# Optimization experiments

Measured on AMD Instinct MI355X. Metric: run time of the kernel, lower is better.

The kernel has to match this reference:

```python
import jax, jax.numpy as jnp
import numpy as np

N = 12288   # num_nodes
D = 128     # isize
K_TOP = 31  # k + 1, per top_k(similarities, self.k + 1)


def setup_inputs() -> dict:
    key = jax.random.key(0)
    features = jax.random.normal(key, (N, D), dtype=jnp.float32)
    eye = jnp.eye(D, dtype=jnp.float32)  # param_init: weight <- I, bias <- 0
    return {
        "features": features,
        "W1": eye,
        "b1": jnp.zeros((D,), jnp.float32),
        "W2": eye,
        "b2": jnp.zeros((D,), jnp.float32),
    }


def reference(features, W1, b1, W2, b2):
    # internal_forward: Linear -> ReLU -> Linear (nlayers=2, act='relu')
    h = jax.nn.relu(features @ W1.T + b1)
    h = h @ W2.T + b2
    # F.normalize(h, dim=1, p=2) with eps=1e-12
    hn = h / jnp.maximum(jnp.linalg.norm(h, axis=1, keepdims=True), 1e-12)
    # dense N x N cosine similarity
    sim = hn @ hn.T
    # top_k: keep top (k+1) entries per row, zero elsewhere; then apply_non_linearity='relu'
    vals, idx = jax.lax.top_k(sim, K_TOP)          # [N, K_TOP]
    rows = jnp.arange(sim.shape[0])[:, None]       # [N, 1]
    # relu(sim * mask) == scatter relu(top-k values) into a zero matrix
    out = jnp.zeros_like(sim).at[rows, idx].set(jax.nn.relu(vals))
    return out
```

## Files before the change

### kernel.cpp

```cpp
#include <hip/hip_runtime.h>
#include <stdint.h>
#include <math.h>

#define NN 12288
#define DD 128
#define KTOP 31
#define TILE 128
#define GB (NN / TILE)
#define TCAND 64
#define CCAP 128
#define FUSE_ROWS 6144

typedef __attribute__((ext_vector_type(8))) short bf16x8;
typedef __attribute__((ext_vector_type(4))) float f32x4;

__device__ __forceinline__ unsigned short f2bf(float x) {
  unsigned int u = __float_as_uint(x);
  u += 0x7fffu + ((u >> 16) & 1u);
  return (unsigned short)(u >> 16);
}

__device__ __forceinline__ unsigned umed3(unsigned a, unsigned b, unsigned c) {
  unsigned d;
  asm("v_med3_u32 %0, %1, %2, %3" : "=v"(d) : "v"(a), "v"(b), "v"(c));
  return d;
}

__global__ __launch_bounds__(128)
void wtrans_kernel(const float* __restrict__ W1, const float* __restrict__ W2,
                   float* __restrict__ W1T, float* __restrict__ W2T) {
  const int r = blockIdx.x, c = threadIdx.x;
  W1T[(size_t)c * DD + r] = W1[(size_t)r * DD + c];
  W2T[(size_t)c * DD + r] = W2[(size_t)r * DD + c];
}

__global__ __launch_bounds__(128)
void mlp_norm_kernel(const float* __restrict__ feat,
                     const float* __restrict__ W1T, const float* __restrict__ b1,
                     const float* __restrict__ W2T, const float* __restrict__ b2,
                     double* __restrict__ hn64, unsigned short* __restrict__ hnb) {
  __shared__ double bufA[8][DD];
  __shared__ double bufB[8][DD];
  __shared__ double mnorm[8];
  const int t = threadIdx.x;
  const int row0 = blockIdx.x * 8;

  #pragma unroll
  for (int rr = 0; rr < 8; ++rr)
    bufA[rr][t] = (double)feat[(size_t)(row0 + rr) * DD + t];
  __syncthreads();

  {
    double acc[8] = {0,0,0,0,0,0,0,0};
    for (int k = 0; k < DD; k += 2) {
      double w0 = (double)W1T[(size_t)k * DD + t];
      double w1 = (double)W1T[(size_t)(k + 1) * DD + t];
      #pragma unroll
      for (int rr = 0; rr < 8; ++rr) {
        double2 a2 = *(const double2*)(&bufA[rr][k]);
        acc[rr] = fma(w0, a2.x, acc[rr]);
        acc[rr] = fma(w1, a2.y, acc[rr]);
      }
    }
    double bb = (double)b1[t];
    #pragma unroll
    for (int rr = 0; rr < 8; ++rr)
      bufB[rr][t] = fmax(acc[rr] + bb, 0.0);
  }
  __syncthreads();
  {
    double acc[8] = {0,0,0,0,0,0,0,0};
    for (int k = 0; k < DD; k += 2) {
      double w0 = (double)W2T[(size_t)k * DD + t];
      double w1 = (double)W2T[(size_t)(k + 1) * DD + t];
      #pragma unroll
      for (int rr = 0; rr < 8; ++rr) {
        double2 a2 = *(const double2*)(&bufB[rr][k]);
        acc[rr] = fma(w0, a2.x, acc[rr]);
        acc[rr] = fma(w1, a2.y, acc[rr]);
      }
    }
    double bb = (double)b2[t];
    #pragma unroll
    for (int rr = 0; rr < 8; ++rr)
      bufA[rr][t] = acc[rr] + bb;
  }
  __syncthreads();

  const int lane = t & 63;
  const int w = t >> 6;
  #pragma unroll
  for (int r2 = 0; r2 < 4; ++r2) {
    int rr = w * 4 + r2;
    double x0 = bufA[rr][lane];
    double x1 = bufA[rr][lane + 64];
    double s = x0 * x0 + x1 * x1;
    #pragma unroll
    for (int d = 1; d < 64; d <<= 1)
      s += __shfl_xor(s, d);
    if (lane == 0) mnorm[rr] = fmax(sqrt(s), 1e-12);
  }
  __syncthreads();
  #pragma unroll
  for (int rr = 0; rr < 8; ++rr) {
    double v = bufA[rr][t] / mnorm[rr];
    hn64[(size_t)(row0 + rr) * DD + t] = v;
    hnb[(size_t)(row0 + rr) * DD + t] = f2bf((float)v);
  }
}

__device__ __forceinline__ int lunit(int c, int r, int q) {
  return c * 512 + r * 4 + ((q + (r >> 1)) & 3);
}

__global__ __launch_bounds__(256)
void gemm_kernel(const unsigned short* __restrict__ hnb,
                 unsigned short* __restrict__ simmat) {
  __shared__ __attribute__((aligned(16))) unsigned short At[16384];
  __shared__ __attribute__((aligned(16))) unsigned short Bt[16384];
  const int t = threadIdx.x;
  const int lane = t & 63;
  const int wv = t >> 6;
  const int bi = blockIdx.x / GB, bj = blockIdx.x % GB;
  const int r0 = bi * TILE, c0 = bj * TILE;

  #pragma unroll
  for (int i = 0; i < 8; ++i) {
    int u = i * 256 + t;
    int c = u >> 9, r = (u >> 2) & 127, g = u & 3;
    int q = (g - (r >> 1)) & 3;
    uint4 v = *(const uint4*)(hnb + (size_t)(r0 + r) * DD + c * 32 + q * 8);
    *(uint4*)(At + u * 8) = v;
  }
  #pragma unroll
  for (int i = 0; i < 8; ++i) {
    int u = i * 256 + t;
    int c = u >> 9, r = (u >> 2) & 127, g = u & 3;
    int q = (g - (r >> 1)) & 3;
    uint4 v = *(const uint4*)(hnb + (size_t)(c0 + r) * DD + c * 32 + q * 8);
    *(uint4*)(Bt + u * 8) = v;
  }
  __syncthreads();

  const int wr = (wv >> 1) * 64;
  const int wc = (wv & 1) * 64;
  const int m = lane & 15, quad = lane >> 4;

  f32x4 acc[4][4] = {};
  #pragma unroll
  for (int kc = 0; kc < 4; ++kc) {
    bf16x8 a[4], b[4];
    #pragma unroll
    for (int i = 0; i < 4; ++i)
      a[i] = *(const bf16x8*)(At + lunit(kc, wr + i * 16 + m, quad) * 8);
    #pragma unroll
    for (int j = 0; j < 4; ++j)
      b[j] = *(const bf16x8*)(Bt + lunit(kc, wc + j * 16 + m, quad) * 8);
    #pragma unroll
    for (int i = 0; i < 4; ++i)
      #pragma unroll
      for (int j = 0; j < 4; ++j)
        acc[i][j] = __builtin_amdgcn_mfma_f32_16x16x32_bf16(a[i], b[j], acc[i][j], 0, 0, 0);
  }

  const bool evenl = !(lane & 1);
  #pragma unroll
  for (int i = 0; i < 4; ++i)
    #pragma unroll
    for (int j = 0; j < 4; ++j)
      #pragma unroll
      for (int r = 0; r < 4; ++r) {
        float v = acc[i][j][r];
        float v2 = __shfl_xor(v, 1);
        if (evenl) {
          unsigned int pk = (unsigned int)f2bf(v) | ((unsigned int)f2bf(v2) << 16);
          int R = r0 + wr + i * 16 + quad * 4 + r;
          int C = c0 + wc + j * 16 + m;
          *(unsigned int*)(simmat + (size_t)R * NN + C) = pk;
        }
      }
}

#define PINS(P) { \
  const unsigned p_ = (P); \
  _Pragma("unroll") \
  for (int i_ = 0; i_ < 7; ++i_) \
    L[i_] = umed3(p_, L[i_], L[i_ + 1]); \
  L[7] = L[7] > p_ ? L[7] : p_; }

__global__ __launch_bounds__(256)
void scan_rescore_kernel(const unsigned short* __restrict__ simmat,
                         const double* __restrict__ hn64,
                         float* __restrict__ resval, int* __restrict__ rescol,
                         float* __restrict__ out) {
  __shared__ unsigned scand[4][CCAP];
  __shared__ double cres[4][CCAP];
  const int t = threadIdx.x, lane = t & 63, wv = t >> 6;
  const int row = blockIdx.x * 4 + wv;
  const unsigned short* srow = simmat + (size_t)row * NN;

  unsigned L[8] = {0, 0, 0, 0, 0, 0, 0, 0};
  for (int it = 0; it < NN / 512; ++it) {
    uint4 pk = *(const uint4*)(srow + it * 512 + lane * 8);
    const unsigned cb = it * 512 + lane * 8;
    unsigned wds[4] = {pk.x, pk.y, pk.z, pk.w};
    #pragma unroll
    for (int q = 0; q < 4; ++q) {
      unsigned b0 = wds[q] & 0xFFFFu, b1v = wds[q] >> 16;
      unsigned s0 = (b0 & 0x8000u) ? 0u : b0;
      unsigned s1 = (b1v & 0x8000u) ? 0u : b1v;
      unsigned p0 = (s0 << 16) | (cb + 2 * q);
      unsigned p1 = (s1 << 16) | (cb + 2 * q + 1);
      PINS(p0)
      PINS(p1)
    }
  }

  unsigned lo = 0, hi = 0xFFFFu;
  while (lo < hi) {
    unsigned mid = (lo + hi + 1) >> 1;
    int c = 0;
    #pragma unroll
    for (int i = 0; i < 8; ++i) c += (int)((L[i] >> 16) >= mid);
    #pragma unroll
    for (int d = 1; d < 64; d <<= 1) c += __shfl_xor(c, d);
    if (c >= TCAND) lo = mid; else hi = mid - 1;
  }
  const unsigned thr = lo;

  int cl = 0;
  #pragma unroll
  for (int i = 0; i < 8; ++i) cl += (int)((L[i] >> 16) >= thr);
  int pre = cl;
  #pragma unroll
  for (int d = 1; d < 64; d <<= 1) {
    int y = __shfl_up(pre, d);
    if (lane >= d) pre += y;
  }
  const int total = __shfl(pre, 63);
  const int nc = total < CCAP ? total : CCAP;
  int slot = pre - cl;
  #pragma unroll
  for (int i = 0; i < 8; ++i) {
    if ((L[i] >> 16) >= thr) {
      if (slot < CCAP) scand[wv][slot] = L[i];
      ++slot;
    }
  }
  __syncthreads();

  const double* arow = hn64 + (size_t)row * DD;
  const int hl = lane >> 5;
  const int kl = (lane & 31) * 4;
  const double a0 = arow[kl], a1 = arow[kl + 1], a2 = arow[kl + 2], a3 = arow[kl + 3];
  const int ng = (nc + 1) >> 1;
  for (int g = 0; g < ng; ++g) {
    const int ci = 2 * g + hl;
    double partial = 0.0;
    if (ci < nc) {
      const int col = (int)(scand[wv][ci] & 0xFFFFu);
      const double* brow = hn64 + (size_t)col * DD + kl;
      double2 b01 = *(const double2*)(brow);
      double2 b23 = *(const double2*)(brow + 2);
      partial = fma(a0, b01.x, fma(a1, b01.y, fma(a2, b23.x, a3 * b23.y)));
    }
    #pragma unroll
    for (int d = 1; d < 32; d <<= 1)
      partial += __shfl_xor(partial, d);
    if ((lane & 31) == 0 && ci < nc) cres[wv][ci] = partial;
  }
  double rv0 = -1.0e300, rv1 = -1.0e300;
  int rc0 = 0x7fffffff, rc1 = 0x7fffffff;
  if (lane < nc) {
    rv0 = cres[wv][lane];
    rc0 = (int)(scand[wv][lane] & 0xFFFFu);
  }
  if (lane + 64 < nc) {
    rv1 = cres[wv][lane + 64];
    rc1 = (int)(scand[wv][lane + 64] & 0xFFFFu);
  }

  const bool fuse = (row < FUSE_ROWS);
  float fkv = 0.0f; int fkc = 0;
  for (int itk = 0; itk < KTOP; ++itk) {
    bool f = (rv0 > rv1) || (rv0 == rv1 && rc0 < rc1);
    double bv = f ? rv0 : rv1;
    int bc = f ? rc0 : rc1;
    #pragma unroll
    for (int d = 1; d < 64; d <<= 1) {
      double ov = __shfl_xor(bv, d);
      int    oc = __shfl_xor(bc, d);
      bool tk = (ov > bv) || (ov == bv && oc < bc);
      bv = tk ? ov : bv;
      bc = tk ? oc : bc;
    }
    if (lane == itk) {
      float ovv = (float)fmax(bv, 0.0);
      fkv = ovv; fkc = bc;
      if (!fuse) {
        resval[(size_t)row * KTOP + itk] = ovv;
        rescol[(size_t)row * KTOP + itk] = bc;
      }
    }
    if (rv0 == bv && rc0 == bc) rv0 = -1.0e300;
    else if (rv1 == bv && rc1 == bc) rv1 = -1.0e300;
  }

  if (fuse) {
    f32x4* orow = (f32x4*)(out + (size_t)row * NN);
    const f32x4 z = {0.0f, 0.0f, 0.0f, 0.0f};
    #pragma unroll
    for (int i = 0; i < NN / 4 / 64; ++i)
      __builtin_nontemporal_store(z, &orow[i * 64 + lane]);
    __syncthreads();
    if (lane < KTOP) out[(size_t)row * NN + fkc] = fkv;
  }
}

__global__ __launch_bounds__(256)
void emit_kernel(const float* __restrict__ resval, const int* __restrict__ rescol,
                 float* __restrict__ out) {
  const int row = blockIdx.x + FUSE_ROWS, t = threadIdx.x;
  float v = 0.0f; int c = 0;
  if (t < KTOP) {
    v = resval[(size_t)row * KTOP + t];
    c = rescol[(size_t)row * KTOP + t];
  }
  f32x4* orow = (f32x4*)(out + (size_t)row * NN);
  const f32x4 z = {0.0f, 0.0f, 0.0f, 0.0f};
  #pragma unroll
  for (int i = 0; i < NN / 4 / 256; ++i)
    __builtin_nontemporal_store(z, &orow[i * 256 + t]);
  __syncthreads();
  if (t < KTOP) out[(size_t)row * NN + c] = v;
}

extern "C" void kernel_launch(void* const* d_in, const int* in_sizes, int n_in,
                              void* d_out, int out_size, void* d_ws, size_t ws_size,
                              hipStream_t stream) {
  const float* feat = (const float*)d_in[0];
  const float* W1 = (const float*)d_in[1];
  const float* b1 = (const float*)d_in[2];
  const float* W2 = (const float*)d_in[3];
  const float* b2 = (const float*)d_in[4];
  float* out = (float*)d_out;

  double* hn64 = (double*)d_ws;
  unsigned short* hnb = (unsigned short*)(hn64 + (size_t)NN * DD);
  float* resval = (float*)(hnb + (size_t)NN * DD);
  int* rescol = (int*)(resval + (size_t)NN * KTOP);
  float* W1T = (float*)(rescol + (size_t)NN * KTOP);
  float* W2T = W1T + DD * DD;

  unsigned short* simmat = (unsigned short*)((char*)d_out + (size_t)NN * NN * 2);

  wtrans_kernel<<<DD, DD, 0, stream>>>(W1, W2, W1T, W2T);
  mlp_norm_kernel<<<NN / 8, 128, 0, stream>>>(feat, W1T, b1, W2T, b2, hn64, hnb);
  gemm_kernel<<<GB * GB, 256, 0, stream>>>(hnb, simmat);
  scan_rescore_kernel<<<NN / 4, 256, 0, stream>>>(simmat, hn64, resval, rescol, out);
  emit_kernel<<<NN - FUSE_ROWS, 256, 0, stream>>>(resval, rescol, out);
}
```

Measured before the change: 948.3 us.

## Fuse similarity GEMM with streaming top-k selection and output zeroing

Replaces the separate bf16 similarity GEMM, scan/rescore and emit kernels with one fused kernel. Each block owns 16 rows, computes similarity tiles with MFMA directly in registers, and feeds each value into a per-lane 16-deep med3 insertion list. Zeroing of the output is interleaved with the GEMM loop. This removes the round trip of the full N×N bf16 similarity matrix through memory. The cost is that every block re-reads all of hnb from global memory/L2 without LDS reuse, and the deeper per-lane lists add VALU work per element.

New measurement: 1.001 ms. +5.5%, slower.

```diff
diff --git a/kernel.cpp b/kernel.cpp
--- a/kernel.cpp
+++ b/kernel.cpp
@@ -5,11 +5,12 @@
 #define NN 12288
 #define DD 128
 #define KTOP 31
-#define TILE 128
-#define GB (NN / TILE)
+#define GB 96
 #define TCAND 64
 #define CCAP 128
-#define FUSE_ROWS 6144
+#define RPB 16
+#define LDEP 16
+#define KBS 260
 
 typedef __attribute__((ext_vector_type(8))) short bf16x8;
 typedef __attribute__((ext_vector_type(4))) float f32x4;
@@ -25,6 +26,13 @@
   asm("v_med3_u32 %0, %1, %2, %3" : "=v"(d) : "v"(a), "v"(b), "v"(c));
   return d;
 }
+
+#define PINS(P) { \
+  const unsigned p_ = (P); \
+  _Pragma("unroll") \
+  for (int i_ = 0; i_ < LDEP - 1; ++i_) \
+    L[i_] = umed3(p_, L[i_], L[i_ + 1]); \
+  L[LDEP - 1] = L[LDEP - 1] > p_ ? L[LDEP - 1] : p_; }
 
 __global__ __launch_bounds__(128)
 void wtrans_kernel(const float* __restrict__ W1, const float* __restrict__ W2,
@@ -109,230 +117,147 @@
   }
 }
 
-__device__ __forceinline__ int lunit(int c, int r, int q) {
-  return c * 512 + r * 4 + ((q + (r >> 1)) & 3);
-}
-
 __global__ __launch_bounds__(256)
-void gemm_kernel(const unsigned short* __restrict__ hnb,
-                 unsigned short* __restrict__ simmat) {
-  __shared__ __attribute__((aligned(16))) unsigned short At[16384];
-  __shared__ __attribute__((aligned(16))) unsigned short Bt[16384];
-  const int t = threadIdx.x;
-  const int lane = t & 63;
-  const int wv = t >> 6;
-  const int bi = blockIdx.x / GB, bj = blockIdx.x % GB;
-  const int r0 = bi * TILE, c0 = bj * TILE;
-
-  #pragma unroll
-  for (int i = 0; i < 8; ++i) {
-    int u = i * 256 + t;
-    int c = u >> 9, r = (u >> 2) & 127, g = u & 3;
-    int q = (g - (r >> 1)) & 3;
-    uint4 v = *(const uint4*)(hnb + (size_t)(r0 + r) * DD + c * 32 + q * 8);
-    *(uint4*)(At + u * 8) = v;
-  }
-  #pragma unroll
-  for (int i = 0; i < 8; ++i) {
-    int u = i * 256 + t;
-    int c = u >> 9, r = (u >> 2) & 127, g = u & 3;
-    int q = (g - (r >> 1)) & 3;
-    uint4 v = *(const uint4*)(hnb + (size_t)(c0 + r) * DD + c * 32 + q * 8);
-    *(uint4*)(Bt + u * 8) = v;
-  }
-  __syncthreads();
-
-  const int wr = (wv >> 1) * 64;
-  const int wc = (wv & 1) * 64;
-  const int m = lane & 15, quad = lane >> 4;
-
-  f32x4 acc[4][4] = {};
-  #pragma unroll
-  for (int kc = 0; kc < 4; ++kc) {
-    bf16x8 a[4], b[4];
-    #pragma unroll
-    for (int i = 0; i < 4; ++i)
-      a[i] = *(const bf16x8*)(At + lunit(kc, wr + i * 16 + m, quad) * 8);
-    #pragma unroll
-    for (int j = 0; j < 4; ++j)
-      b[j] = *(const bf16x8*)(Bt + lunit(kc, wc + j * 16 + m, quad) * 8);
-    #pragma unroll
-    for (int i = 0; i < 4; ++i)
-      #pragma unroll
-      for (int j = 0; j < 4; ++j)
-        acc[i][j] = __builtin_amdgcn_mfma_f32_16x16x32_bf16(a[i], b[j], acc[i][j], 0, 0, 0);
-  }
-
-  const bool evenl = !(lane & 1);
-  #pragma unroll
-  for (int i = 0; i < 4; ++i)
-    #pragma unroll
-    for (int j = 0; j < 4; ++j)
-      #pragma unroll
-      for (int r = 0; r < 4; ++r) {
-        float v = acc[i][j][r];
-        float v2 = __shfl_xor(v, 1);
-        if (evenl) {
-          unsigned int pk = (unsigned int)f2bf(v) | ((unsigned int)f2bf(v2) << 16);
-          int R = r0 + wr + i * 16 + quad * 4 + r;
-          int C = c0 + wc + j * 16 + m;
-          *(unsigned int*)(simmat + (size_t)R * NN + C) = pk;
-        }
-      }
-}
-
-#define PINS(P) { \
-  const unsigned p_ = (P); \
-  _Pragma("unroll") \
-  for (int i_ = 0; i_ < 7; ++i_) \
-    L[i_] = umed3(p_, L[i_], L[i_ + 1]); \
-  L[7] = L[7] > p_ ? L[7] : p_; }
-
-__global__ __launch_bounds__(256)
-void scan_rescore_kernel(const unsigned short* __restrict__ simmat,
-                         const double* __restrict__ hn64,
-                         float* __restrict__ resval, int* __restrict__ rescol,
-                         float* __restrict__ out) {
+void fused_kernel(const unsigned short* __restrict__ hnb,
+                  const double* __restrict__ hn64,
+                  float* __restrict__ out) {
+  __shared__ unsigned keybuf[RPB][KBS];
   __shared__ unsigned scand[4][CCAP];
   __shared__ double cres[4][CCAP];
   const int t = threadIdx.x, lane = t & 63, wv = t >> 6;
-  const int row = blockIdx.x * 4 + wv;
-  const unsigned short* srow = simmat + (size_t)row * NN;
-
-  unsigned L[8] = {0, 0, 0, 0, 0, 0, 0, 0};
-  for (int it = 0; it < NN / 512; ++it) {
-    uint4 pk = *(const uint4*)(srow + it * 512 + lane * 8);
-    const unsigned cb = it * 512 + lane * 8;
-    unsigned wds[4] = {pk.x, pk.y, pk.z, pk.w};
-    #pragma unroll
-    for (int q = 0; q < 4; ++q) {
-      unsigned b0 = wds[q] & 0xFFFFu, b1v = wds[q] >> 16;
-      unsigned s0 = (b0 & 0x8000u) ? 0u : b0;
-      unsigned s1 = (b1v & 0x8000u) ? 0u : b1v;
-      unsigned p0 = (s0 << 16) | (cb + 2 * q);
-      unsigned p1 = (s1 << 16) | (cb + 2 * q + 1);
-      PINS(p0)
-      PINS(p1)
-    }
-  }
-
-  unsigned lo = 0, hi = 0xFFFFu;
-  while (lo < hi) {
-    unsigned mid = (lo + hi + 1) >> 1;
-    int c = 0;
-    #pragma unroll
-    for (int i = 0; i < 8; ++i) c += (int)((L[i] >> 16) >= mid);
-    #pragma unroll
-    for (int d = 1; d < 64; d <<= 1) c += __shfl_xor(c, d);
-    if (c >= TCAND) lo = mid; else hi = mid - 1;
-  }
-  const unsigned thr = lo;
-
-  int cl = 0;
-  #pragma unroll
-  for (int i = 0; i < 8; ++i) cl += (int)((L[i] >> 16) >= thr);
-  int pre = cl;
-  #pragma unroll
-  for (int d = 1; d < 64; d <<= 1) {
-    int y = __shfl_up(pre, d);
-    if (lane >= d) pre += y;
-  }
-  const int total = __shfl(pre, 63);
-  const int nc = total < CCAP ? total : CCAP;
-  int slot = pre - cl;
-  #pragma unroll
-  for (int i = 0; i < 8; ++i) {
-    if ((L[i] >> 16) >= thr) {
-      if (slot < CCAP) scand[wv][slot] = L[i];
-      ++slot;
-    }
-  }
-  __syncthreads();
-
-  const double* arow = hn64 + (size_t)row * DD;
-  const int hl = lane >> 5;
-  const int kl = (lane & 31) * 4;
-  const double a0 = arow[kl], a1 = arow[kl + 1], a2 = arow[kl + 2], a3 = arow[kl + 3];
-  const int ng = (nc + 1) >> 1;
-  for (int g = 0; g < ng; ++g) {
-    const int ci = 2 * g + hl;
-    double partial = 0.0;
-    if (ci < nc) {
-      const int col = (int)(scand[wv][ci] & 0xFFFFu);
-      const double* brow = hn64 + (size_t)col * DD + kl;
-      double2 b01 = *(const double2*)(brow);
-      double2 b23 = *(const double2*)(brow + 2);
-      partial = fma(a0, b01.x, fma(a1, b01.y, fma(a2, b23.x, a3 * b23.y)));
-    }
-    #pragma unroll
-    for (int d = 1; d < 32; d <<= 1)
-      partial += __shfl_xor(partial, d);
-    if ((lane & 31) == 0 && ci < nc) cres[wv][ci] = partial;
-  }
-  double rv0 = -1.0e300, rv1 = -1.0e300;
-  int rc0 = 0x7fffffff, rc1 = 0x7fffffff;
-  if (lane < nc) {
-    rv0 = cres[wv][lane];
-    rc0 = (int)(scand[wv][lane] & 0xFFFFu);
-  }
-  if (lane + 64 < nc) {
-    rv1 = cres[wv][lane + 64];
-    rc1 = (int)(scand[wv][lane + 64] & 0xFFFFu);
-  }
-
-  const bool fuse = (row < FUSE_ROWS);
-  float fkv = 0.0f; int fkc = 0;
-  for (int itk = 0; itk < KTOP; ++itk) {
-    bool f = (rv0 > rv1) || (rv0 == rv1 && rc0 < rc1);
-    double bv = f ? rv0 : rv1;
-    int bc = f ? rc0 : rc1;
+  const int m = lane & 15, quad = lane >> 4;
+  const int row0 = blockIdx.x * RPB;
+
+  bf16x8 afrag[4];
+  #pragma unroll
+  for (int kc = 0; kc < 4; ++kc)
+    afrag[kc] = *(const bf16x8*)(hnb + (size_t)(row0 + m) * DD + kc * 32 + quad * 8);
+
+  unsigned L[LDEP];
+  #pragma unroll
+  for (int i = 0; i < LDEP; ++i) L[i] = 0;
+
+  f32x4* outz = (f32x4*)(out + (size_t)(row0 + wv * 4) * NN);
+  const f32x4 z = {0.0f, 0.0f, 0.0f, 0.0f};
+
+  for (int tile = 0; tile < GB; ++tile) {
+    const int cb = tile * 128 + wv * 32;
+    f32x4 acc0 = {0.0f, 0.0f, 0.0f, 0.0f};
+    f32x4 acc1 = {0.0f, 0.0f, 0.0f, 0.0f};
+    #pragma unroll
+    for (int kc = 0; kc < 4; ++kc) {
+      bf16x8 b0 = *(const bf16x8*)(hnb + (size_t)(cb + m) * DD + kc * 32 + quad * 8);
+      bf16x8 b1 = *(const bf16x8*)(hnb + (size_t)(cb + 16 + m) * DD + kc * 32 + quad * 8);
+      acc0 = __builtin_amdgcn_mfma_f32_16x16x32_bf16(b0, afrag[kc], acc0, 0, 0, 0);
+      acc1 = __builtin_amdgcn_mfma_f32_16x16x32_bf16(b1, afrag[kc], acc1, 0, 0, 0);
+    }
+    __builtin_nontemporal_store(z, &outz[tile * 128 + lane]);
+    __builtin_nontemporal_store(z, &outz[tile * 128 + 64 + lane]);
+    #pragma unroll
+    for (int r = 0; r < 4; ++r) {
+      {
+        unsigned bf = f2bf(acc0[r]);
+        unsigned s = (bf & 0x8000u) ? 0u : bf;
+        unsigned p = (s << 16) | (unsigned)(cb + quad * 4 + r);
+        PINS(p)
+      }
+      {
+        unsigned bf = f2bf(acc1[r]);
+        unsigned s = (bf & 0x8000u) ? 0u : bf;
+        unsigned p = (s << 16) | (unsigned)(cb + 16 + quad * 4 + r);
+        PINS(p)
+      }
+    }
+  }
+
+  #pragma unroll
+  for (int d = 0; d < LDEP; ++d)
+    keybuf[m][(wv * 4 + quad) * LDEP + d] = L[d];
+  __syncthreads();
+
+  for (int ii = 0; ii < 4; ++ii) {
+    const int lr = wv * 4 + ii;
+    const int grow = row0 + lr;
+    uint4 kk = *(const uint4*)(&keybuf[lr][lane * 4]);
+    unsigned k4[4] = {kk.x, kk.y, kk.z, kk.w};
+
+    unsigned lo = 0, hi = 0xFFFFu;
+    while (lo < hi) {
+      unsigned mid = (lo + hi + 1) >> 1;
+      int c = 0;
+      #pragma unroll
+      for (int i = 0; i < 4; ++i) c += (int)((k4[i] >> 16) >= mid);
+      #pragma unroll
+      for (int d = 1; d < 64; d <<= 1) c += __shfl_xor(c, d);
+      if (c >= TCAND) lo = mid; else hi = mid - 1;
+    }
+    const unsigned thr = lo;
+
+    int cl = 0;
+    #pragma unroll
+    for (int i = 0; i < 4; ++i) cl += (int)((k4[i] >> 16) >= thr);
+    int pre = cl;
     #pragma unroll
     for (int d = 1; d < 64; d <<= 1) {
-      double ov = __shfl_xor(bv, d);
-      int    oc = __shfl_xor(bc, d);
-      bool tk = (ov > bv) || (ov == bv && oc < bc);
-      bv = tk ? ov : bv;
-      bc = tk ? oc : bc;
-    }
-    if (lane == itk) {
-      float ovv = (float)fmax(bv, 0.0);
-      fkv = ovv; fkc = bc;
-      if (!fuse) {
-        resval[(size_t)row * KTOP + itk] = ovv;
-        rescol[(size_t)row * KTOP + itk] = bc;
-      }
-    }
-    if (rv0 == bv && rc0 == bc) rv0 = -1.0e300;
-    else if (rv1 == bv && rc1 == bc) rv1 = -1.0e300;
-  }
-
-  if (fuse) {
-    f32x4* orow = (f32x4*)(out + (size_t)row * NN);
-    const f32x4 z = {0.0f, 0.0f, 0.0f, 0.0f};
-    #pragma unroll
-    for (int i = 0; i < NN / 4 / 64; ++i)
-      __builtin_nontemporal_store(z, &orow[i * 64 + lane]);
-    __syncthreads();
-    if (lane < KTOP) out[(size_t)row * NN + fkc] = fkv;
-  }
-}
-
-__global__ __launch_bounds__(256)
-void emit_kernel(const float* __restrict__ resval, const int* __restrict__ rescol,
-                 float* __restrict__ out) {
-  const int row = blockIdx.x + FUSE_ROWS, t = threadIdx.x;
-  float v = 0.0f; int c = 0;
-  if (t < KTOP) {
-    v = resval[(size_t)row * KTOP + t];
-    c = rescol[(size_t)row * KTOP + t];
-  }
-  f32x4* orow = (f32x4*)(out + (size_t)row * NN);
-  const f32x4 z = {0.0f, 0.0f, 0.0f, 0.0f};
-  #pragma unroll
-  for (int i = 0; i < NN / 4 / 256; ++i)
-    __builtin_nontemporal_store(z, &orow[i * 256 + t]);
-  __syncthreads();
-  if (t < KTOP) out[(size_t)row * NN + c] = v;
+      int y = __shfl_up(pre, d);
+      if (lane >= d) pre += y;
+    }
+    const int total = __shfl(pre, 63);
+    const int nc = total < CCAP ? total : CCAP;
+    int slot = pre - cl;
+    #pragma unroll
+    for (int i = 0; i < 4; ++i) {
+      if ((k4[i] >> 16) >= thr) {
+        if (slot < CCAP) scand[wv][slot] = k4[i];
+        ++slot;
+      }
+    }
+
+    const double* arow = hn64 + (size_t)grow * DD;
+    const int hl = lane >> 5;
+    const int kl = (lane & 31) * 4;
+    const double a0 = arow[kl], a1 = arow[kl + 1], a2 = arow[kl + 2], a3 = arow[kl + 3];
+    const int ng = (nc + 1) >> 1;
+    for (int g = 0; g < ng; ++g) {
+      const int ci = 2 * g + hl;
+      double partial = 0.0;
+      if (ci < nc) {
+        const int col = (int)(scand[wv][ci] & 0xFFFFu);
+        const double* brow = hn64 + (size_t)col * DD + kl;
+        double2 b01 = *(const double2*)(brow);
+        double2 b23 = *(const double2*)(brow + 2);
+        partial = fma(a0, b01.x, fma(a1, b01.y, fma(a2, b23.x, a3 * b23.y)));
+      }
+      #pragma unroll
+      for (int d = 1; d < 32; d <<= 1)
+        partial += __shfl_xor(partial, d);
+      if ((lane & 31) == 0 && ci < nc) cres[wv][ci] = partial;
+    }
+    double rv0 = -1.0e300, rv1 = -1.0e300;
+    int rc0 = 0x7fffffff, rc1 = 0x7fffffff;
+    if (lane < nc)      { rv0 = cres[wv][lane];      rc0 = (int)(scand[wv][lane] & 0xFFFFu); }
+    if (lane + 64 < nc) { rv1 = cres[wv][lane + 64]; rc1 = (int)(scand[wv][lane + 64] & 0xFFFFu); }
+
+    float fkv = 0.0f; int fkc = 0;
+    for (int itk = 0; itk < KTOP; ++itk) {
+      bool f = (rv0 > rv1) || (rv0 == rv1 && rc0 < rc1);
+      double bv = f ? rv0 : rv1;
+      int bc = f ? rc0 : rc1;
+      #pragma unroll
+      for (int d = 1; d < 64; d <<= 1) {
+        double ov = __shfl_xor(bv, d);
+        int    oc = __shfl_xor(bc, d);
+        bool tk = (ov > bv) || (ov == bv && oc < bc);
+        bv = tk ? ov : bv;
+        bc = tk ? oc : bc;
+      }
+      if (lane == itk) { fkv = (float)fmax(bv, 0.0); fkc = bc; }
+      if (rv0 == bv && rc0 == bc) rv0 = -1.0e300;
+      else if (rv1 == bv && rc1 == bc) rv1 = -1.0e300;
+    }
+    asm volatile("s_waitcnt vmcnt(0)" ::: "memory");
+    if (lane < KTOP) out[(size_t)grow * NN + fkc] = fkv;
+  }
 }
 
 extern "C" void kernel_launch(void* const* d_in, const int* in_sizes, int n_in,
@@ -347,16 +272,10 @@
 
   double* hn64 = (double*)d_ws;
   unsigned short* hnb = (unsigned short*)(hn64 + (size_t)NN * DD);
-  float* resval = (float*)(hnb + (size_t)NN * DD);
-  int* rescol = (int*)(resval + (size_t)NN * KTOP);
-  float* W1T = (float*)(rescol + (size_t)NN * KTOP);
+  float* W1T = (float*)(hnb + (size_t)NN * DD);
   float* W2T = W1T + DD * DD;
-
-  unsigned short* simmat = (unsigned short*)((char*)d_out + (size_t)NN * NN * 2);
 
   wtrans_kernel<<<DD, DD, 0, stream>>>(W1, W2, W1T, W2T);
   mlp_norm_kernel<<<NN / 8, 128, 0, stream>>>(feat, W1T, b1, W2T, b2, hn64, hnb);
-  gemm_kernel<<<GB * GB, 256, 0, stream>>>(hnb, simmat);
-  scan_rescore_kernel<<<NN / 4, 256, 0, stream>>>(simmat, hn64, resval, rescol, out);
-  emit_kernel<<<NN - FUSE_ROWS, 256, 0, stream>>>(resval, rescol, out);
-}
+  fused_kernel<<<NN / RPB, 256, 0, stream>>>(hnb, hn64, out);
+}
```
